# Kernel optimization log

Hardware: AMD Instinct MI355X
Metric: run time of the kernel (lower is better)

## Reference

```python
import jax, jax.numpy as jnp
import numpy as np

D_MODEL = 2048
D_INNER = 2 * D_MODEL      # expand=2
D_STATE = 16
D_CONV = 4
DT_RANK = D_MODEL // 16    # ceil(2048/16)=128
BATCH, SEQLEN = 2, 1024


def setup_inputs() -> dict:
    key = jax.random.key(0)
    ks = jax.random.split(key, 10)
    s = 0.02
    inp = {
        "hidden_states": jax.random.normal(ks[0], (BATCH, SEQLEN, D_MODEL), jnp.float32),
        "in_proj_w": jax.random.normal(ks[1], (2 * D_INNER, D_MODEL), jnp.float32) * s,
        "conv_w": jax.random.normal(ks[2], (D_INNER, D_CONV), jnp.float32) * s,
        "conv_b": jax.random.normal(ks[3], (D_INNER,), jnp.float32) * s,
        "x_proj_w": jax.random.normal(ks[4], (DT_RANK + 2 * D_STATE, D_INNER), jnp.float32) * s,
        "dt_proj_w": jax.random.normal(ks[5], (D_INNER, DT_RANK), jnp.float32) * s,
        "dt_proj_b": jax.random.normal(ks[6], (D_INNER,), jnp.float32) * 0.1,
        "A_log": jnp.log(jnp.tile(jnp.arange(1, D_STATE + 1, dtype=jnp.float32), (D_INNER, 1))),
        "D": jnp.ones((D_INNER,), jnp.float32),
        "out_proj_w": jax.random.normal(ks[7], (D_MODEL, D_INNER), jnp.float32) * s,
    }
    return inp


def _mamba_forward(hidden_states, in_proj_w, conv_w, conv_b, x_proj_w,
                   dt_proj_w, dt_proj_b, A_log, D, out_proj_w):
    B, L, _ = hidden_states.shape
    # input projection -> x, z  (each [B, L, D_INNER])
    xz = jnp.einsum('bld,ed->ble', hidden_states, in_proj_w)
    x, z = jnp.split(xz, 2, axis=-1)
    # causal depthwise conv1d (kernel D_CONV) + SiLU
    x_pad = jnp.pad(x, ((0, 0), (D_CONV - 1, 0), (0, 0)))
    windows = jnp.stack([x_pad[:, k:k + L, :] for k in range(D_CONV)], axis=-1)  # [B,L,D,K]
    x_conv = jnp.einsum('bldk,dk->bld', windows, conv_w) + conv_b
    x_act = jax.nn.silu(x_conv)
    # data-dependent SSM parameters
    x_dbl = jnp.einsum('bld,ed->ble', x_act, x_proj_w)
    dt, Bc, Cc = jnp.split(x_dbl, [DT_RANK, DT_RANK + D_STATE], axis=-1)
    dt = jax.nn.softplus(jnp.einsum('blr,dr->bld', dt, dt_proj_w) + dt_proj_b)  # [B,L,D_INNER]
    A = -jnp.exp(A_log)  # [D_INNER, D_STATE]

    # selective scan over time (carry h: [B, D_INNER, D_STATE])
    def step(h, inp):
        x_t, dt_t, B_t, C_t = inp  # [B,D],[B,D],[B,N],[B,N]
        dA = jnp.exp(dt_t[:, :, None] * A[None])          # [B,D,N]
        dBx = dt_t[:, :, None] * B_t[:, None, :] * x_t[:, :, None]
        h = h * dA + dBx
        y = jnp.einsum('bdn,bn->bd', h, C_t)
        return h, y

    xs = (x_act.transpose(1, 0, 2), dt.transpose(1, 0, 2),
          Bc.transpose(1, 0, 2), Cc.transpose(1, 0, 2))
    h0 = jnp.zeros((B, D_INNER, D_STATE), x_act.dtype)
    _, ys = jax.lax.scan(step, h0, xs)          # [L,B,D_INNER]
    y = ys.transpose(1, 0, 2) + x_act * D       # skip connection D*x
    y = y * jax.nn.silu(z)                      # gating
    return jnp.einsum('bld,md->blm', y, out_proj_w)


def reference(hidden_states, in_proj_w, conv_w, conv_b, x_proj_w,
              dt_proj_w, dt_proj_b, A_log, D, out_proj_w):
    return _mamba_forward(hidden_states, in_proj_w, conv_w, conv_b, x_proj_w,
                          dt_proj_w, dt_proj_b, A_log, D, out_proj_w)
```

## Files before the change

kernel.cpp:

```cpp
#include <hip/hip_runtime.h>
#include <cstdint>
#include <cstddef>

#define D_MODEL 2048
#define D_INNER 4096
#define D_IN2   8192
#define D_STATE 16
#define D_CONVK 4
#define DT_RANK 128
#define BATCH   2
#define SEQLEN  1024
#define BL      (BATCH*SEQLEN)
#define XDBL_N  (DT_RANK + 2*D_STATE)
#define XPW_NPAD 256
#define XPROJ_SPLITS 8
#define OUT_SPLITS 2

#define NCHUNK  16
#define LCHUNK  (SEQLEN/NCHUNK)
#define CHW     (BATCH*D_INNER*D_STATE)

#define NB_HID   2048
#define NB_IPW   8192
#define NB_XPW   320
#define NB_XPWZ  192
#define NB_DTW   256
#define NB_OPW   4096
#define NB_XDBLZ 320

typedef short  s8v  __attribute__((ext_vector_type(8)));
typedef float  f4v  __attribute__((ext_vector_type(4)));

__device__ __forceinline__ float softplus_f(float v) {
    return (v > 20.f) ? v : log1pf(__expf(v));
}
__device__ __forceinline__ float silu_f(float v) {
    return v / (1.f + __expf(-v));
}
__device__ __forceinline__ float bf2f(short s) {
    return __uint_as_float(((uint32_t)(uint16_t)s) << 16);
}
__device__ __forceinline__ uint16_t f2bf(float f) {
    uint32_t u = __float_as_uint(f);
    return (uint16_t)((u + 0x7FFFu + ((u >> 16) & 1u)) >> 16);
}
__device__ __forceinline__ uint32_t packbf(float lo, float hi) {
    return ((uint32_t)f2bf(hi) << 16) | (uint32_t)f2bf(lo);
}
__device__ __forceinline__ float quad_sum(float p) {
    p += __int_as_float(__builtin_amdgcn_update_dpp(
            0, __float_as_int(p), 0xB1, 0xF, 0xF, true));
    p += __int_as_float(__builtin_amdgcn_update_dpp(
            0, __float_as_int(p), 0x4E, 0xF, 0xF, true));
    return p;
}

#define GLD16(gp, lp)                                                          \
    __builtin_amdgcn_global_load_lds(                                          \
        (const __attribute__((address_space(1))) void*)(gp),                   \
        (__attribute__((address_space(3))) void*)(lp), 16, 0, 0)

__global__ __launch_bounds__(256)
void k_cast_all(const float* __restrict__ s0, uint32_t* __restrict__ d0,
                const float* __restrict__ s1, uint32_t* __restrict__ d1,
                const float* __restrict__ s2, uint32_t* __restrict__ d2,
                const float* __restrict__ s3, uint32_t* __restrict__ d3,
                const float* __restrict__ s4, uint32_t* __restrict__ d4,
                uint32_t* __restrict__ z0, uint32_t* __restrict__ z1)
{
    int blk = blockIdx.x;
    const float* src = nullptr; uint32_t* dst; int base; int zero = 0;
    if      (blk < NB_HID) { src = s0; dst = d0; base = blk; }
    else if ((blk -= NB_HID)  < NB_IPW)  { src = s1; dst = d1; base = blk; }
    else if ((blk -= NB_IPW)  < NB_XPW)  { src = s2; dst = d2; base = blk; }
    else if ((blk -= NB_XPW)  < NB_XPWZ) { dst = z0; base = blk; zero = 1; }
    else if ((blk -= NB_XPWZ) < NB_DTW)  { src = s3; dst = d3; base = blk; }
    else if ((blk -= NB_DTW)  < NB_OPW)  { src = s4; dst = d4; base = blk; }
    else                                 { dst = z1; base = blk - NB_OPW; zero = 1; }
    const int i = base * 256 + threadIdx.x;
    if (zero) { ((uint4*)dst)[i] = make_uint4(0u, 0u, 0u, 0u); return; }
    const float4 a = ((const float4*)src)[i * 2];
    const float4 b = ((const float4*)src)[i * 2 + 1];
    uint4 o;
    o.x = packbf(a.x, a.y); o.y = packbf(a.z, a.w);
    o.z = packbf(b.x, b.y); o.w = packbf(b.z, b.w);
    ((uint4*)dst)[i] = o;
}

template<int EPI>
__device__ __forceinline__
void gemm_body(const short* __restrict__ A, int lda,
               const short* __restrict__ W, int ldw,
               void* __restrict__ Cv, int ldc, int M, int kchunk)
{
    constexpr int SMEM_BYTES = (EPI == 2) ? 34816 : (EPI == 0) ? 33792 : 32768;
    __shared__ __align__(16) char smem[SMEM_BYTES];
    short* sA = (short*)smem;
    short* sW = (short*)(smem + 16384);

    const int tid = threadIdx.x;
    const int w   = tid >> 6;
    const int L   = tid & 63;
    const int bm  = blockIdx.y * 128;
    const int bn  = blockIdx.x * 128;
    const int k0  = blockIdx.z * kchunk;

    const int rsub = L >> 3;
    const int c8   = (((L & 7) - rsub) & 7) * 8;
    const short* Ag[4]; const short* Wg[4];
#pragma unroll
    for (int j = 0; j < 4; j++) {
        Ag[j] = A + (size_t)(bm + w * 32 + j * 8 + rsub) * lda + c8 + k0;
        Wg[j] = W + (size_t)(bn + w * 32 + j * 8 + rsub) * ldw + c8 + k0;
    }

    const int wm = (w >> 1) * 64;
    const int wn = (w & 1) * 64;
    const int cl = L & 15;
    const int qd = L >> 4;

    f4v acc[4][4];
#pragma unroll
    for (int i = 0; i < 4; i++)
#pragma unroll
        for (int j = 0; j < 4; j++) acc[i][j] = (f4v){0.f, 0.f, 0.f, 0.f};

    for (int k = 0; k < kchunk; k += 64) {
#pragma unroll
        for (int j = 0; j < 4; j++)
            GLD16(Ag[j] + k, &sA[(w * 32 + j * 8) * 64]);
#pragma unroll
        for (int j = 0; j < 4; j++)
            GLD16(Wg[j] + k, &sW[(w * 32 + j * 8) * 64]);
        __syncthreads();
#pragma unroll
        for (int kk = 0; kk < 2; kk++) {
            const int sl = ((kk * 4 + qd + cl) & 7) * 8;
            s8v a[4], b[4];
#pragma unroll
            for (int mt = 0; mt < 4; mt++)
                a[mt] = *(const s8v*)&sA[(wm + mt * 16 + cl) * 64 + sl];
#pragma unroll
            for (int nt = 0; nt < 4; nt++)
                b[nt] = *(const s8v*)&sW[(wn + nt * 16 + cl) * 64 + sl];
#pragma unroll
            for (int mt = 0; mt < 4; mt++)
#pragma unroll
                for (int nt = 0; nt < 4; nt++)
                    acc[mt][nt] = __builtin_amdgcn_mfma_f32_16x16x32_bf16(
                        a[mt], b[nt], acc[mt][nt], 0, 0, 0);
        }
        __syncthreads();
    }

    if constexpr (EPI == 2) {
        ushort (*sC)[136] = (ushort(*)[136])smem;
        short* Cs = (short*)Cv;
#pragma unroll
        for (int mt = 0; mt < 4; mt++)
#pragma unroll
            for (int nt = 0; nt < 4; nt++)
#pragma unroll
                for (int r = 0; r < 4; r++)
                    sC[wm + mt * 16 + qd * 4 + r][wn + nt * 16 + cl] =
                        (ushort)f2bf(acc[mt][nt][r]);
        __syncthreads();
#pragma unroll
        for (int it = 0; it < 8; it++) {
            const int idx = it * 256 + tid;
            const int row = idx >> 4;
            const int c8s = (idx & 15) * 8;
            *(uint4*)&Cs[(size_t)(bm + row) * ldc + bn + c8s] =
                *(const uint4*)&sC[row][c8s];
        }
    } else if constexpr (EPI == 0) {
        float (*sC)[132] = (float(*)[132])smem;
        float* Cf = (float*)Cv + (size_t)blockIdx.z * M * ldc;
#pragma unroll
        for (int half = 0; half < 2; half++) {
            __syncthreads();
            if (wm == half * 64) {
#pragma unroll
                for (int mt = 0; mt < 4; mt++)
#pragma unroll
                    for (int nt = 0; nt < 4; nt++)
#pragma unroll
                        for (int r = 0; r < 4; r++)
                            sC[mt * 16 + qd * 4 + r][wn + nt * 16 + cl] =
                                acc[mt][nt][r];
            }
            __syncthreads();
#pragma unroll
            for (int it = 0; it < 8; it++) {
                const int f4  = it * 256 + tid;
                const int row = f4 >> 5;
                const int c4  = (f4 & 31) * 4;
                const float4 v = *(const float4*)&sC[row][c4];
                *(float4*)&Cf[(size_t)(bm + half * 64 + row) * ldc + bn + c4] = v;
            }
        }
    } else {
        float* Cf = (float*)Cv;
#pragma unroll
        for (int mt = 0; mt < 4; mt++) {
            const int row0 = bm + wm + mt * 16 + qd * 4;
#pragma unroll
            for (int nt = 0; nt < 4; nt++) {
                const int col = bn + wn + nt * 16 + cl;
                if (col >= XDBL_N) continue;
#pragma unroll
                for (int r = 0; r < 4; r++)
                    atomicAdd(&Cf[(size_t)(row0 + r) * ldc + col], acc[mt][nt][r]);
            }
        }
    }
}

__global__ __launch_bounds__(256)
void k_gemm_inproj(const short* A, const short* W, short* C)
{ gemm_body<2>(A, D_MODEL, W, D_MODEL, C, D_IN2, BL, D_MODEL); }

__global__ __launch_bounds__(256)
void k_gemm_xproj(const short* A, const short* W, float* C)
{ gemm_body<3>(A, D_INNER, W, D_INNER, C, XDBL_N, BL, D_INNER / XPROJ_SPLITS); }

__global__ __launch_bounds__(256)
void k_gemm_outproj(const short* A, const short* W, float* C)
{ gemm_body<0>(A, D_INNER, W, D_INNER, C, D_MODEL, BL, D_INNER / OUT_SPLITS); }

__global__ __launch_bounds__(256)
void k_gemm_dt(const float* __restrict__ Af, const short* __restrict__ W,
               float* __restrict__ C)
{
    __shared__ __align__(16) char smem[65536];
    short* sA = (short*)smem;
    short* sW = (short*)(smem + 32768);

    const int tid = threadIdx.x;
    const int w   = tid >> 6;
    const int L   = tid & 63;
    const int bm  = blockIdx.y * 128;
    const int bn  = blockIdx.x * 128;

#pragma unroll
    for (int ci = 0; ci < 8; ci++) {
        const int c_lin = tid * 8 + ci;
        const int r = c_lin >> 4;
        const int c = c_lin & 15;
        const float* src = Af + (size_t)(bm + r) * XDBL_N + c * 8;
        const float4 u = *(const float4*)src;
        const float4 v = *(const float4*)(src + 4);
        const int half = c >> 3, cc = c & 7;
        const int slot = (cc + r) & 7;
        uint4 o;
        o.x = packbf(u.x, u.y); o.y = packbf(u.z, u.w);
        o.z = packbf(v.x, v.y); o.w = packbf(v.z, v.w);
        *(uint4*)&sA[half * 8192 + r * 64 + slot * 8] = o;
    }
    const int rsub = L >> 3;
    const int c8   = (((L & 7) - rsub) & 7) * 8;
#pragma unroll
    for (int half = 0; half < 2; half++)
#pragma unroll
        for (int j = 0; j < 4; j++)
            GLD16(W + (size_t)(bn + w * 32 + j * 8 + rsub) * DT_RANK + half * 64 + c8,
                  &sW[half * 8192 + (w * 32 + j * 8) * 64]);
    __syncthreads();

    const int wm = (w >> 1) * 64;
    const int wn = (w & 1) * 64;
    const int cl = L & 15;
    const int qd = L >> 4;

    f4v acc[4][4];
#pragma unroll
    for (int i = 0; i < 4; i++)
#pragma unroll
        for (int j = 0; j < 4; j++) acc[i][j] = (f4v){0.f, 0.f, 0.f, 0.f};

#pragma unroll
    for (int ks = 0; ks < 4; ks++) {
        const int half = ks >> 1;
        const int sl = (((ks & 1) * 4 + qd + cl) & 7) * 8;
        s8v a[4], b[4];
#pragma unroll
        for (int mt = 0; mt < 4; mt++)
            a[mt] = *(const s8v*)&sA[half * 8192 + (wm + mt * 16 + cl) * 64 + sl];
#pragma unroll
        for (int nt = 0; nt < 4; nt++)
            b[nt] = *(const s8v*)&sW[half * 8192 + (wn + nt * 16 + cl) * 64 + sl];
#pragma unroll
        for (int mt = 0; mt < 4; mt++)
#pragma unroll
            for (int nt = 0; nt < 4; nt++)
                acc[mt][nt] = __builtin_amdgcn_mfma_f32_16x16x32_bf16(
                    a[mt], b[nt], acc[mt][nt], 0, 0, 0);
    }

    __syncthreads();
    float (*sC)[132] = (float(*)[132])smem;
#pragma unroll
    for (int half = 0; half < 2; half++) {
        __syncthreads();
        if (wm == half * 64) {
#pragma unroll
            for (int mt = 0; mt < 4; mt++)
#pragma unroll
                for (int nt = 0; nt < 4; nt++)
#pragma unroll
                    for (int r = 0; r < 4; r++)
                        sC[mt * 16 + qd * 4 + r][wn + nt * 16 + cl] =
                            acc[mt][nt][r];
        }
        __syncthreads();
#pragma unroll
        for (int it = 0; it < 8; it++) {
            const int f4  = it * 256 + tid;
            const int row = f4 >> 5;
            const int c4  = (f4 & 31) * 4;
            const float4 v = *(const float4*)&sC[row][c4];
            *(float4*)&C[(size_t)(bm + half * 64 + row) * D_INNER + bn + c4] = v;
        }
    }
}

__global__ __launch_bounds__(256)
void k_reduce_out(const float* __restrict__ P, float* __restrict__ out)
{
    const int i = blockIdx.x * 256 + threadIdx.x;
    const float4 a = ((const float4*)P)[i];
    const float4 b = ((const float4*)(P + (size_t)BL * D_MODEL))[i];
    ((float4*)out)[i] = make_float4(a.x + b.x, a.y + b.y, a.z + b.z, a.w + b.w);
}

__global__ __launch_bounds__(256)
void k_conv(const short* __restrict__ xz_bf, const float* __restrict__ cw,
            const float* __restrict__ cb, short* __restrict__ x_bf)
{
    const int idx = blockIdx.x * 256 + threadIdx.x;
    const int d  = idx & (D_INNER - 1);
    const int bl = idx >> 12;
    const int l  = bl & (SEQLEN - 1);
    const int b  = bl >> 10;
    const short* xb = xz_bf + (size_t)b * SEQLEN * D_IN2 + d;
    float acc = cb[d];
#pragma unroll
    for (int k = 0; k < D_CONVK; k++) {
        const int ll = l + k - (D_CONVK - 1);
        if (ll >= 0) acc = fmaf(bf2f(xb[(size_t)ll * D_IN2]), cw[d * D_CONVK + k], acc);
    }
    x_bf[idx] = (short)f2bf(silu_f(acc));
}

__global__ __launch_bounds__(256)
void k_scan_p1(const short* __restrict__ x_bf, const float* __restrict__ dtr,
               const float* __restrict__ dtb, const float* __restrict__ xdbl,
               const float* __restrict__ A_log,
               float* __restrict__ h_end, float* __restrict__ Pprod)
{
    const int c   = blockIdx.y;
    const int ch0 = blockIdx.x * 64;
    const int b   = ch0 >> 12;
    const int d0  = ch0 & (D_INNER - 1);
    const int tid = threadIdx.x;
    const int g   = tid >> 2;
    const int q   = tid & 3;
    const int d   = d0 + g;

    const float4 Al = *(const float4*)&A_log[(d << 4) + (q << 2)];
    float An[4] = {-__expf(Al.x), -__expf(Al.y), -__expf(Al.z), -__expf(Al.w)};
    float h[4]  = {0.f, 0.f, 0.f, 0.f};
    float Pp[4] = {1.f, 1.f, 1.f, 1.f};

    __shared__ float s_x [16][68];
    __shared__ float s_dt[16][68];
    __shared__ float s_B [16][20];

    const int lt  = tid >> 4;
    const int ld4 = (tid & 15) * 4;
    const float4 bb = *(const float4*)&dtb[d0 + ld4];

    for (int sub = 0; sub < LCHUNK / 16; sub++) {
        const int l0 = c * LCHUNK + sub * 16;
        const size_t bl = (size_t)(b * SEQLEN + l0 + lt);
        __syncthreads();
        {
            const short4 sx = *(const short4*)&x_bf[bl * D_INNER + d0 + ld4];
            const float4 dv = *(const float4*)&dtr[bl * D_INNER + d0 + ld4];
            *(float4*)&s_x [lt][ld4] =
                make_float4(bf2f(sx.x), bf2f(sx.y), bf2f(sx.z), bf2f(sx.w));
            *(float4*)&s_dt[lt][ld4] = make_float4(
                softplus_f(dv.x + bb.x), softplus_f(dv.y + bb.y),
                softplus_f(dv.z + bb.z), softplus_f(dv.w + bb.w));
            if (tid < 64) {
                const int t2 = tid >> 2, k = (tid & 3) * 4;
                const size_t bl2 = (size_t)(b * SEQLEN + l0 + t2);
                *(float4*)&s_B[t2][k] =
                    *(const float4*)&xdbl[bl2 * XDBL_N + DT_RANK + k];
            }
        }
        __syncthreads();
#pragma unroll
        for (int t = 0; t < 16; t++) {
            const float xv  = s_x [t][g];
            const float dtv = s_dt[t][g];
            const float4 Bq = *(const float4*)&s_B[t][q * 4];
            const float Bv[4] = {Bq.x, Bq.y, Bq.z, Bq.w};
            const float dtx = dtv * xv;
#pragma unroll
            for (int j = 0; j < 4; j++) {
                const float dA = __expf(dtv * An[j]);
                h[j]  = fmaf(h[j], dA, dtx * Bv[j]);
                Pp[j] *= dA;
            }
        }
    }
    const size_t i0 = (size_t)c * CHW + (((size_t)(b * D_INNER + d)) << 4) + (q << 2);
    *(float4*)&h_end[i0] = make_float4(h[0], h[1], h[2], h[3]);
    *(float4*)&Pprod[i0] = make_float4(Pp[0], Pp[1], Pp[2], Pp[3]);
}

__global__ __launch_bounds__(256)
void k_scan_p3(const short* __restrict__ x_bf, short* __restrict__ y_bf,
               const float* __restrict__ dtr, const float* __restrict__ dtb,
               const float* __restrict__ xdbl,
               const short* __restrict__ xz_bf, const float* __restrict__ A_log,
               const float* __restrict__ Dvec,
               const float* __restrict__ h_end, const float* __restrict__ Pbuf)
{
    const int c   = blockIdx.y;
    const int ch0 = blockIdx.x * 64;
    const int b   = ch0 >> 12;
    const int d0  = ch0 & (D_INNER - 1);
    const int tid = threadIdx.x;
    const int g   = tid >> 2;
    const int q   = tid & 3;
    const int d   = d0 + g;

    const float4 Al = *(const float4*)&A_log[(d << 4) + (q << 2)];
    float An[4] = {-__expf(Al.x), -__expf(Al.y), -__expf(Al.z), -__expf(Al.w)};
    const float Dd = Dvec[d];

    float h[4] = {0.f, 0.f, 0.f, 0.f};
    const size_t base = (((size_t)(b * D_INNER + d)) << 4) + (q << 2);
    for (int j = 0; j < c; j++) {
        const float4 he = *(const float4*)&h_end[(size_t)j * CHW + base];
        const float4 Pp = *(const float4*)&Pbuf [(size_t)j * CHW + base];
        h[0] = fmaf(Pp.x, h[0], he.x);
        h[1] = fmaf(Pp.y, h[1], he.y);
        h[2] = fmaf(Pp.z, h[2], he.z);
        h[3] = fmaf(Pp.w, h[3], he.w);
    }

    __shared__ float s_x [16][68];
    __shared__ float s_dt[16][68];
    __shared__ float s_z [16][68];
    __shared__ float s_B [16][20];
    __shared__ float s_C [16][20];

    const int lt  = tid >> 4;
    const int ld4 = (tid & 15) * 4;
    const float4 bb = *(const float4*)&dtb[d0 + ld4];

    for (int sub = 0; sub < LCHUNK / 16; sub++) {
        const int l0 = c * LCHUNK + sub * 16;
        const size_t bl = (size_t)(b * SEQLEN + l0 + lt);
        __syncthreads();
        {
            const short4 sx = *(const short4*)&x_bf[bl * D_INNER + d0 + ld4];
            const float4 dv = *(const float4*)&dtr[bl * D_INNER + d0 + ld4];
            const short4 zv = *(const short4*)&xz_bf[bl * D_IN2 + D_INNER + d0 + ld4];
            *(float4*)&s_x [lt][ld4] =
                make_float4(bf2f(sx.x), bf2f(sx.y), bf2f(sx.z), bf2f(sx.w));
            *(float4*)&s_dt[lt][ld4] = make_float4(
                softplus_f(dv.x + bb.x), softplus_f(dv.y + bb.y),
                softplus_f(dv.z + bb.z), softplus_f(dv.w + bb.w));
            *(float4*)&s_z [lt][ld4] =
                make_float4(bf2f(zv.x), bf2f(zv.y), bf2f(zv.z), bf2f(zv.w));
            if (tid < 128) {
                const int t2 = (tid & 63) >> 2, k = (tid & 3) * 4;
                const size_t bl2 = (size_t)(b * SEQLEN + l0 + t2);
                const int off = (tid < 64) ? 0 : D_STATE;
                const float4 v =
                    *(const float4*)&xdbl[bl2 * XDBL_N + DT_RANK + off + k];
                if (tid < 64) *(float4*)&s_B[t2][k] = v;
                else          *(float4*)&s_C[t2][k] = v;
            }
        }
        __syncthreads();
        const size_t orow = (size_t)(b * SEQLEN + l0);
#pragma unroll
        for (int t = 0; t < 16; t++) {
            const float xv  = s_x [t][g];
            const float dtv = s_dt[t][g];
            const float4 Bq = *(const float4*)&s_B[t][q * 4];
            const float4 Cq = *(const float4*)&s_C[t][q * 4];
            const float Bv[4] = {Bq.x, Bq.y, Bq.z, Bq.w};
            const float Cv[4] = {Cq.x, Cq.y, Cq.z, Cq.w};
            const float dtx = dtv * xv;
            float p = 0.f;
#pragma unroll
            for (int j = 0; j < 4; j++) {
                const float dA = __expf(dtv * An[j]);
                h[j] = fmaf(h[j], dA, dtx * Bv[j]);
                p = fmaf(h[j], Cv[j], p);
            }
            p = quad_sum(p);
            if (q == 0) {
                const float yv = fmaf(xv, Dd, p) * silu_f(s_z[t][g]);
                y_bf[(orow + t) * D_INNER + d] = (short)f2bf(yv);
            }
        }
    }
}

extern "C" void kernel_launch(void* const* d_in, const int* in_sizes, int n_in,
                              void* d_out, int out_size, void* d_ws, size_t ws_size,
                              hipStream_t stream)
{
    const float* hidden     = (const float*)d_in[0];
    const float* in_proj_w  = (const float*)d_in[1];
    const float* conv_w     = (const float*)d_in[2];
    const float* conv_b     = (const float*)d_in[3];
    const float* x_proj_w   = (const float*)d_in[4];
    const float* dt_proj_w  = (const float*)d_in[5];
    const float* dt_proj_b  = (const float*)d_in[6];
    const float* A_log      = (const float*)d_in[7];
    const float* Dvec       = (const float*)d_in[8];
    const float* out_proj_w = (const float*)d_in[9];
    float* out = (float*)d_out;

    const size_t MB = 1ull << 20;
    char* ws = (char*)d_ws;
    short* xz_bf   = (short*)(ws);
    short* x_bf    = (short*)(ws + 32 * MB);
    short* ipw_bf  = (short*)(ws + 48 * MB);
    short* y_bf    = (short*)(ws + 48 * MB);
    float* h_end   = (float*)(ws + 64 * MB);
    float* Pbuf    = (float*)(ws + 72 * MB);
    short* hid_bf  = (short*)(ws + 80 * MB);
    short* opw_bf  = (short*)(ws + 88 * MB);
    float* dt_raw  = (float*)(ws + 104 * MB);
    float* op_part = (float*)(ws + 104 * MB);
    short* xpw_bf  = (short*)(ws + 136 * MB);
    short* dtw_bf  = (short*)(ws + 138 * MB);
    float* xdbl_f  = (float*)(ws + 139 * MB);

    const dim3 blk(256);

    k_cast_all<<<dim3(NB_HID + NB_IPW + NB_XPW + NB_XPWZ + NB_DTW + NB_OPW + NB_XDBLZ),
                blk, 0, stream>>>(
        hidden, (uint32_t*)hid_bf, in_proj_w, (uint32_t*)ipw_bf,
        x_proj_w, (uint32_t*)xpw_bf, dt_proj_w, (uint32_t*)dtw_bf,
        out_proj_w, (uint32_t*)opw_bf,
        (uint32_t*)(xpw_bf + (size_t)XDBL_N * D_INNER),
        (uint32_t*)xdbl_f);

    k_gemm_inproj<<<dim3(D_IN2 / 128, BL / 128, 1), blk, 0, stream>>>(
        hid_bf, ipw_bf, xz_bf);

    k_conv<<<dim3((BL * D_INNER) / 256), blk, 0, stream>>>(
        xz_bf, conv_w, conv_b, x_bf);

    k_gemm_xproj<<<dim3(XPW_NPAD / 128, BL / 128, XPROJ_SPLITS), blk, 0, stream>>>(
        x_bf, xpw_bf, xdbl_f);

    k_gemm_dt<<<dim3(D_INNER / 128, BL / 128), blk, 0, stream>>>(
        xdbl_f, dtw_bf, dt_raw);

    k_scan_p1<<<dim3(BATCH * D_INNER / 64, NCHUNK - 1), blk, 0, stream>>>(
        x_bf, dt_raw, dt_proj_b, xdbl_f, A_log, h_end, Pbuf);
    k_scan_p3<<<dim3(BATCH * D_INNER / 64, NCHUNK), blk, 0, stream>>>(
        x_bf, y_bf, dt_raw, dt_proj_b, xdbl_f, xz_bf, A_log, Dvec, h_end, Pbuf);

    k_gemm_outproj<<<dim3(D_MODEL / 128, BL / 128, OUT_SPLITS), blk, 0, stream>>>(
        y_bf, opw_bf, op_part);
    k_reduce_out<<<dim3(BL * D_MODEL / 4 / 256), blk, 0, stream>>>(op_part, out);
}
```

Baseline: 461.1 us.

## Prefetch next scan sub-tile into registers and reorder p3 grid by chunk

Both scan kernels now load the next 16-step sub-tile of x, dt, z and B/C into registers while computing the current one, which hides global load latency behind the recurrence. The chunk-prefix combine in p3 is unrolled by four so that eight loads are in flight at once. The p3 grid is transposed so that blocks for the same channel group but different chunks are scheduled next to each other, which may improve cache reuse of h_end and Pbuf. Both kernels also get a min-blocks launch bound of 8, which could force register spills.

New measurement: 486.4 us. 5.5% more time.

```diff
diff --git a/kernel.cpp b/kernel.cpp
--- a/kernel.cpp
+++ b/kernel.cpp
@@ -352,7 +352,7 @@
     x_bf[idx] = (short)f2bf(silu_f(acc));
 }
 
-__global__ __launch_bounds__(256)
+__global__ __launch_bounds__(256, 8)
 void k_scan_p1(const short* __restrict__ x_bf, const float* __restrict__ dtr,
                const float* __restrict__ dtb, const float* __restrict__ xdbl,
                const float* __restrict__ A_log,
@@ -378,28 +378,38 @@
 
     const int lt  = tid >> 4;
     const int ld4 = (tid & 15) * 4;
+    const int t2  = tid >> 2;
+    const int k4  = (tid & 3) * 4;
     const float4 bb = *(const float4*)&dtb[d0 + ld4];
 
+    short4 rx; float4 rdt, rB;
+    {
+        const size_t bl_ = (size_t)(b * SEQLEN + c * LCHUNK + lt);
+        rx  = *(const short4*)&x_bf[bl_ * D_INNER + d0 + ld4];
+        rdt = *(const float4*)&dtr [bl_ * D_INNER + d0 + ld4];
+        if (tid < 64)
+            rB = *(const float4*)&xdbl[(size_t)(b * SEQLEN + c * LCHUNK + t2)
+                                       * XDBL_N + DT_RANK + k4];
+    }
+
     for (int sub = 0; sub < LCHUNK / 16; sub++) {
-        const int l0 = c * LCHUNK + sub * 16;
-        const size_t bl = (size_t)(b * SEQLEN + l0 + lt);
-        __syncthreads();
-        {
-            const short4 sx = *(const short4*)&x_bf[bl * D_INNER + d0 + ld4];
-            const float4 dv = *(const float4*)&dtr[bl * D_INNER + d0 + ld4];
-            *(float4*)&s_x [lt][ld4] =
-                make_float4(bf2f(sx.x), bf2f(sx.y), bf2f(sx.z), bf2f(sx.w));
-            *(float4*)&s_dt[lt][ld4] = make_float4(
-                softplus_f(dv.x + bb.x), softplus_f(dv.y + bb.y),
-                softplus_f(dv.z + bb.z), softplus_f(dv.w + bb.w));
-            if (tid < 64) {
-                const int t2 = tid >> 2, k = (tid & 3) * 4;
-                const size_t bl2 = (size_t)(b * SEQLEN + l0 + t2);
-                *(float4*)&s_B[t2][k] =
-                    *(const float4*)&xdbl[bl2 * XDBL_N + DT_RANK + k];
-            }
-        }
-        __syncthreads();
+        __syncthreads();
+        *(float4*)&s_x [lt][ld4] =
+            make_float4(bf2f(rx.x), bf2f(rx.y), bf2f(rx.z), bf2f(rx.w));
+        *(float4*)&s_dt[lt][ld4] = make_float4(
+            softplus_f(rdt.x + bb.x), softplus_f(rdt.y + bb.y),
+            softplus_f(rdt.z + bb.z), softplus_f(rdt.w + bb.w));
+        if (tid < 64) *(float4*)&s_B[t2][k4] = rB;
+        __syncthreads();
+        if (sub + 1 < LCHUNK / 16) {
+            const int l0n = c * LCHUNK + (sub + 1) * 16;
+            const size_t bl_ = (size_t)(b * SEQLEN + l0n + lt);
+            rx  = *(const short4*)&x_bf[bl_ * D_INNER + d0 + ld4];
+            rdt = *(const float4*)&dtr [bl_ * D_INNER + d0 + ld4];
+            if (tid < 64)
+                rB = *(const float4*)&xdbl[(size_t)(b * SEQLEN + l0n + t2)
+                                           * XDBL_N + DT_RANK + k4];
+        }
 #pragma unroll
         for (int t = 0; t < 16; t++) {
             const float xv  = s_x [t][g];
@@ -420,7 +430,7 @@
     *(float4*)&Pprod[i0] = make_float4(Pp[0], Pp[1], Pp[2], Pp[3]);
 }
 
-__global__ __launch_bounds__(256)
+__global__ __launch_bounds__(256, 8)
 void k_scan_p3(const short* __restrict__ x_bf, short* __restrict__ y_bf,
                const float* __restrict__ dtr, const float* __restrict__ dtb,
                const float* __restrict__ xdbl,
@@ -428,8 +438,8 @@
                const float* __restrict__ Dvec,
                const float* __restrict__ h_end, const float* __restrict__ Pbuf)
 {
-    const int c   = blockIdx.y;
-    const int ch0 = blockIdx.x * 64;
+    const int c   = blockIdx.x;
+    const int ch0 = blockIdx.y * 64;
     const int b   = ch0 >> 12;
     const int d0  = ch0 & (D_INNER - 1);
     const int tid = threadIdx.x;
@@ -443,13 +453,31 @@
 
     float h[4] = {0.f, 0.f, 0.f, 0.f};
     const size_t base = (((size_t)(b * D_INNER + d)) << 4) + (q << 2);
-    for (int j = 0; j < c; j++) {
-        const float4 he = *(const float4*)&h_end[(size_t)j * CHW + base];
-        const float4 Pp = *(const float4*)&Pbuf [(size_t)j * CHW + base];
-        h[0] = fmaf(Pp.x, h[0], he.x);
-        h[1] = fmaf(Pp.y, h[1], he.y);
-        h[2] = fmaf(Pp.z, h[2], he.z);
-        h[3] = fmaf(Pp.w, h[3], he.w);
+    {
+        int j = 0;
+        for (; j + 4 <= c; j += 4) {
+            float4 he[4], Pq[4];
+#pragma unroll
+            for (int u = 0; u < 4; u++) {
+                he[u] = *(const float4*)&h_end[(size_t)(j + u) * CHW + base];
+                Pq[u] = *(const float4*)&Pbuf [(size_t)(j + u) * CHW + base];
+            }
+#pragma unroll
+            for (int u = 0; u < 4; u++) {
+                h[0] = fmaf(Pq[u].x, h[0], he[u].x);
+                h[1] = fmaf(Pq[u].y, h[1], he[u].y);
+                h[2] = fmaf(Pq[u].z, h[2], he[u].z);
+                h[3] = fmaf(Pq[u].w, h[3], he[u].w);
+            }
+        }
+        for (; j < c; j++) {
+            const float4 he = *(const float4*)&h_end[(size_t)j * CHW + base];
+            const float4 Pq = *(const float4*)&Pbuf [(size_t)j * CHW + base];
+            h[0] = fmaf(Pq.x, h[0], he.x);
+            h[1] = fmaf(Pq.y, h[1], he.y);
+            h[2] = fmaf(Pq.z, h[2], he.z);
+            h[3] = fmaf(Pq.w, h[3], he.w);
+        }
     }
 
     __shared__ float s_x [16][68];
@@ -460,34 +488,47 @@
 
     const int lt  = tid >> 4;
     const int ld4 = (tid & 15) * 4;
+    const int t2  = (tid & 63) >> 2;
+    const int k4  = (tid & 3) * 4;
+    const int offc = (tid < 64) ? 0 : D_STATE;
     const float4 bb = *(const float4*)&dtb[d0 + ld4];
+
+    short4 rx, rz; float4 rdt, rBC;
+    {
+        const size_t bl_ = (size_t)(b * SEQLEN + c * LCHUNK + lt);
+        rx  = *(const short4*)&x_bf[bl_ * D_INNER + d0 + ld4];
+        rdt = *(const float4*)&dtr [bl_ * D_INNER + d0 + ld4];
+        rz  = *(const short4*)&xz_bf[bl_ * D_IN2 + D_INNER + d0 + ld4];
+        if (tid < 128)
+            rBC = *(const float4*)&xdbl[(size_t)(b * SEQLEN + c * LCHUNK + t2)
+                                        * XDBL_N + DT_RANK + offc + k4];
+    }
 
     for (int sub = 0; sub < LCHUNK / 16; sub++) {
         const int l0 = c * LCHUNK + sub * 16;
-        const size_t bl = (size_t)(b * SEQLEN + l0 + lt);
-        __syncthreads();
-        {
-            const short4 sx = *(const short4*)&x_bf[bl * D_INNER + d0 + ld4];
-            const float4 dv = *(const float4*)&dtr[bl * D_INNER + d0 + ld4];
-            const short4 zv = *(const short4*)&xz_bf[bl * D_IN2 + D_INNER + d0 + ld4];
-            *(float4*)&s_x [lt][ld4] =
-                make_float4(bf2f(sx.x), bf2f(sx.y), bf2f(sx.z), bf2f(sx.w));
-            *(float4*)&s_dt[lt][ld4] = make_float4(
-                softplus_f(dv.x + bb.x), softplus_f(dv.y + bb.y),
-                softplus_f(dv.z + bb.z), softplus_f(dv.w + bb.w));
-            *(float4*)&s_z [lt][ld4] =
-                make_float4(bf2f(zv.x), bf2f(zv.y), bf2f(zv.z), bf2f(zv.w));
-            if (tid < 128) {
-                const int t2 = (tid & 63) >> 2, k = (tid & 3) * 4;
-                const size_t bl2 = (size_t)(b * SEQLEN + l0 + t2);
-                const int off = (tid < 64) ? 0 : D_STATE;
-                const float4 v =
-                    *(const float4*)&xdbl[bl2 * XDBL_N + DT_RANK + off + k];
-                if (tid < 64) *(float4*)&s_B[t2][k] = v;
-                else          *(float4*)&s_C[t2][k] = v;
-            }
-        }
-        __syncthreads();
+        __syncthreads();
+        *(float4*)&s_x [lt][ld4] =
+            make_float4(bf2f(rx.x), bf2f(rx.y), bf2f(rx.z), bf2f(rx.w));
+        *(float4*)&s_dt[lt][ld4] = make_float4(
+            softplus_f(rdt.x + bb.x), softplus_f(rdt.y + bb.y),
+            softplus_f(rdt.z + bb.z), softplus_f(rdt.w + bb.w));
+        *(float4*)&s_z [lt][ld4] =
+            make_float4(bf2f(rz.x), bf2f(rz.y), bf2f(rz.z), bf2f(rz.w));
+        if (tid < 128) {
+            if (tid < 64) *(float4*)&s_B[t2][k4] = rBC;
+            else          *(float4*)&s_C[t2][k4] = rBC;
+        }
+        __syncthreads();
+        if (sub + 1 < LCHUNK / 16) {
+            const int l0n = l0 + 16;
+            const size_t bl_ = (size_t)(b * SEQLEN + l0n + lt);
+            rx  = *(const short4*)&x_bf[bl_ * D_INNER + d0 + ld4];
+            rdt = *(const float4*)&dtr [bl_ * D_INNER + d0 + ld4];
+            rz  = *(const short4*)&xz_bf[bl_ * D_IN2 + D_INNER + d0 + ld4];
+            if (tid < 128)
+                rBC = *(const float4*)&xdbl[(size_t)(b * SEQLEN + l0n + t2)
+                                            * XDBL_N + DT_RANK + offc + k4];
+        }
         const size_t orow = (size_t)(b * SEQLEN + l0);
 #pragma unroll
         for (int t = 0; t < 16; t++) {
@@ -570,7 +611,7 @@
 
     k_scan_p1<<<dim3(BATCH * D_INNER / 64, NCHUNK - 1), blk, 0, stream>>>(
         x_bf, dt_raw, dt_proj_b, xdbl_f, A_log, h_end, Pbuf);
-    k_scan_p3<<<dim3(BATCH * D_INNER / 64, NCHUNK), blk, 0, stream>>>(
+    k_scan_p3<<<dim3(NCHUNK, BATCH * D_INNER / 64), blk, 0, stream>>>(
         x_bf, y_bf, dt_raw, dt_proj_b, xdbl_f, xz_bf, A_log, Dvec, h_end, Pbuf);
 
     k_gemm_outproj<<<dim3(D_MODEL / 128, BL / 128, OUT_SPLITS), blk, 0, stream>>>(
```
